# Optimization experiments

Measured on AMD Instinct MI355X. Metric: run time of the kernel, lower is better.

Reference implementation:

```python
import jax, jax.numpy as jnp
import numpy as np

TRIANGLE_TABLE = jnp.array([
    [-1,-1,-1,-1,-1,-1],[1,0,2,-1,-1,-1],[4,0,3,-1,-1,-1],[1,4,2,1,3,4],
    [3,1,5,-1,-1,-1],[2,3,0,2,5,3],[1,4,0,1,5,4],[4,2,5,-1,-1,-1],
    [4,5,2,-1,-1,-1],[4,1,0,4,5,1],[3,2,0,3,5,2],[1,3,5,-1,-1,-1],
    [4,1,2,4,3,1],[3,0,4,-1,-1,-1],[2,0,1,-1,-1,-1],[-1,-1,-1,-1,-1,-1]], dtype=jnp.int32)
NUM_TRI_TABLE = jnp.array([0,1,1,2,1,2,2,1,1,2,2,1,2,1,1,0], dtype=jnp.int32)
BASE_TET_EDGES = jnp.array([0,1,0,2,0,3,1,2,1,3,2,3], dtype=jnp.int32)
N_VERTS, N_TETS = 200_000, 1_000_000


def setup_inputs() -> dict:
    key = jax.random.key(0)
    k1, k2, k3 = jax.random.split(key, 3)
    pos_nx3 = jax.random.normal(k1, (N_VERTS, 3), jnp.float32)
    sdf_n = jax.random.normal(k2, (N_VERTS,), jnp.float32)
    tet_fx4 = jax.random.randint(k3, (N_TETS, 4), 0, N_VERTS, dtype=jnp.int32)
    return {"pos_nx3": pos_nx3, "sdf_n": sdf_n, "tet_fx4": tet_fx4}


def _mt_indices(sdf_n, tet_fx4):
    # Index-only part (torch.no_grad in the original). Dynamic shapes -> eager jax.
    occ_n = sdf_n > 0                              # [N]
    occ_fx4 = occ_n[tet_fx4]                       # [T,4]
    occ_sum = occ_fx4.sum(-1)
    valid = (occ_sum > 0) & (occ_sum < 4)          # surface-crossing tets
    tets_v = tet_fx4[valid]                        # [Tv,4]
    occ_v = occ_fx4[valid]
    # 6 edges per tet, sorted so (min,max) -> dedup identical to torch sort_edges+unique
    all_edges = jnp.sort(tets_v[:, BASE_TET_EDGES].reshape(-1, 2), axis=1)  # [Tv*6,2]
    unique_edges, idx_map = jnp.unique(all_edges, axis=0, return_inverse=True)
    idx_map = idx_map.reshape(-1)
    mask_edges = occ_n[unique_edges].sum(-1) == 1  # exactly one endpoint inside
    # compacting map: -1 for non-crossing edges, running index for crossing ones
    mapping = jnp.where(mask_edges, jnp.cumsum(mask_edges.astype(jnp.int32)) - 1, -1)
    idx_map = mapping[idx_map].reshape(-1, 6)      # [Tv,6] per-tet edge->vertex ids
    interp_v = unique_edges[mask_edges]            # [Ne,2] endpoint indices
    return valid, occ_v, idx_map, interp_v


def _interp_verts(pos, sdf, interp_v):
    e_pos = pos[interp_v]                                   # [Ne,2,3]
    e_sdf = sdf[interp_v] * jnp.array([1.0, -1.0], sdf.dtype)  # [s0,-s1]
    denom = e_sdf.sum(1, keepdims=True)                     # s0 - s1
    w = e_sdf[:, ::-1] / denom                              # [-s1, s0] / (s0-s1)
    return (e_pos * w[..., None]).sum(1)                    # [Ne,3]


def _map_uv(face_gidx, max_idx):
    Ngrid = int(np.ceil(np.sqrt((max_idx + 1) // 2)))
    lin = jnp.linspace(0.0, 1.0 - 1.0 / Ngrid, Ngrid, dtype=jnp.float32)
    tex_y, tex_x = jnp.meshgrid(lin, lin, indexing='ij')
    pad = 0.9 / Ngrid
    uvs = jnp.stack([tex_x, tex_y, tex_x + pad, tex_y,
                     tex_x + pad, tex_y + pad, tex_x, tex_y + pad], axis=-1).reshape(-1, 2)
    tet_raw = face_gidx // 2
    tet_idx = (tet_raw // Ngrid) * Ngrid + tet_raw % Ngrid
    tri_idx = face_gidx % 2
    uv_idx = jnp.stack([tet_idx * 4, tet_idx * 4 + tri_idx + 1,
                        tet_idx * 4 + tri_idx + 2], axis=-1).reshape(-1, 3)
    return uvs, uv_idx


def reference(pos_nx3, sdf_n, tet_fx4):
    valid, occ_v, idx_map, interp_v = _mt_indices(sdf_n, tet_fx4)
    verts = _interp_verts(pos_nx3, sdf_n, interp_v)
    # triangle-table lookup
    v_id = jnp.array([1, 2, 4, 8], jnp.int32)
    tetindex = (occ_v.astype(jnp.int32) * v_id).sum(-1)     # [Tv]
    num_tri = NUM_TRI_TABLE[tetindex]
    m1, m2 = num_tri == 1, num_tri == 2
    faces1 = jnp.take_along_axis(idx_map[m1], TRIANGLE_TABLE[tetindex[m1]][:, :3], axis=1).reshape(-1, 3)
    faces2 = jnp.take_along_axis(idx_map[m2], TRIANGLE_TABLE[tetindex[m2]][:, :6], axis=1).reshape(-1, 3)
    faces = jnp.concatenate([faces1, faces2], axis=0)
    tet_gidx = jnp.nonzero(valid)[0].astype(jnp.int32)
    face_gidx = jnp.concatenate([
        tet_gidx[m1] * 2,
        jnp.stack([tet_gidx[m2] * 2, tet_gidx[m2] * 2 + 1], axis=-1).reshape(-1)], axis=0)
    uvs, uv_idx = _map_uv(face_gidx, tet_fx4.shape[0] * 2)
    return verts, faces, uvs, uv_idx
```

## Files before the change

kernel.cpp:

```cpp
#include <hip/hip_runtime.h>
#include <cmath>

typedef unsigned long long u64;
typedef unsigned int u32;
typedef unsigned char u8;

#define SCAN_BLOCK 256
#define SCAN_ELEMS 8
#define SCAN_TILE (SCAN_BLOCK * SCAN_ELEMS)

#define BIN_SHIFT 9
#define BIN_VR 512
#define TETS_PER_BLOCK 2048

__constant__ int d_NUMTRI[16] = {0,1,1,2,1,2,2,1,1,2,2,1,2,1,1,0};
__constant__ int d_TRI[16][6] = {
 {-1,-1,-1,-1,-1,-1},{1,0,2,-1,-1,-1},{4,0,3,-1,-1,-1},{1,4,2,1,3,4},
 {3,1,5,-1,-1,-1},{2,3,0,2,5,3},{1,4,0,1,5,4},{4,2,5,-1,-1,-1},
 {4,5,2,-1,-1,-1},{4,1,0,4,5,1},{3,2,0,3,5,2},{1,3,5,-1,-1,-1},
 {4,1,2,4,3,1},{3,0,4,-1,-1,-1},{2,0,1,-1,-1,-1},{-1,-1,-1,-1,-1,-1}};
__constant__ int d_E0[6] = {0,0,0,1,1,2};
__constant__ int d_E1[6] = {1,2,3,2,3,3};

template <typename T>
__global__ void scanA_t(const T* in, T* out, int n, T* blockSums) {
    __shared__ T tsum[SCAN_BLOCK];
    int tbase = blockIdx.x * SCAN_TILE + threadIdx.x * SCAN_ELEMS;
    T vals[SCAN_ELEMS];
    T run = 0;
    for (int k = 0; k < SCAN_ELEMS; ++k) {
        int i = tbase + k;
        T v = (i < n) ? in[i] : (T)0;
        vals[k] = run;
        run += v;
    }
    tsum[threadIdx.x] = run;
    __syncthreads();
    for (int off = 1; off < SCAN_BLOCK; off <<= 1) {
        T v = (threadIdx.x >= (unsigned)off) ? tsum[threadIdx.x - off] : (T)0;
        __syncthreads();
        tsum[threadIdx.x] += v;
        __syncthreads();
    }
    T texcl = (threadIdx.x == 0) ? (T)0 : tsum[threadIdx.x - 1];
    for (int k = 0; k < SCAN_ELEMS; ++k) {
        int i = tbase + k;
        if (i < n) out[i] = texcl + vals[k];
    }
    if (threadIdx.x == SCAN_BLOCK - 1) blockSums[blockIdx.x] = tsum[SCAN_BLOCK - 1];
}

template <typename T>
__global__ void scanCf_t(T* out, int n, const T* bs, int nb, T* totalOut) {
    __shared__ T sh[2048];
    for (int i = threadIdx.x; i < 2048; i += 256) sh[i] = (i < nb) ? bs[i] : (T)0;
    __syncthreads();
    for (int off = 1; off < 2048; off <<= 1) {
        T v[8];
        for (int k = 0; k < 8; ++k) {
            int i = threadIdx.x + k * 256;
            v[k] = (i >= off) ? sh[i - off] : (T)0;
        }
        __syncthreads();
        for (int k = 0; k < 8; ++k) sh[threadIdx.x + k * 256] += v[k];
        __syncthreads();
    }
    if (totalOut && blockIdx.x == 0 && threadIdx.x == 0)
        *totalOut = (nb > 0) ? sh[nb - 1] : (T)0;
    T add = (blockIdx.x == 0) ? (T)0 : sh[blockIdx.x - 1];
    int base = blockIdx.x * SCAN_TILE;
    int end = base + SCAN_TILE; if (end > n) end = n;
    for (int i = base + threadIdx.x; i < end; i += SCAN_BLOCK) out[i] += add;
}

__global__ void k_scanA_dual(const u64* in64, u64* out64, int n64, u64* bs64,
                             const u32* in32, u32* out32, int n32, u32* bs32,
                             int nbT) {
    __shared__ u64 tsum[SCAN_BLOCK];
    if ((int)blockIdx.x < nbT) {
        int tbase = blockIdx.x * SCAN_TILE + threadIdx.x * SCAN_ELEMS;
        u64 vals[SCAN_ELEMS]; u64 run = 0;
        for (int k = 0; k < SCAN_ELEMS; ++k) {
            int i = tbase + k;
            u64 v = (i < n64) ? in64[i] : 0ull;
            vals[k] = run; run += v;
        }
        tsum[threadIdx.x] = run;
        __syncthreads();
        for (int off = 1; off < SCAN_BLOCK; off <<= 1) {
            u64 v = (threadIdx.x >= (unsigned)off) ? tsum[threadIdx.x - off] : 0ull;
            __syncthreads();
            tsum[threadIdx.x] += v;
            __syncthreads();
        }
        u64 texcl = (threadIdx.x == 0) ? 0ull : tsum[threadIdx.x - 1];
        for (int k = 0; k < SCAN_ELEMS; ++k) {
            int i = tbase + k;
            if (i < n64) out64[i] = texcl + vals[k];
        }
        if (threadIdx.x == SCAN_BLOCK - 1) bs64[blockIdx.x] = tsum[SCAN_BLOCK - 1];
    } else {
        int blk = (int)blockIdx.x - nbT;
        int tbase = blk * SCAN_TILE + threadIdx.x * SCAN_ELEMS;
        u32 vals[SCAN_ELEMS]; u32 run = 0;
        for (int k = 0; k < SCAN_ELEMS; ++k) {
            int i = tbase + k;
            u32 v = (i < n32) ? in32[i] : 0u;
            vals[k] = run; run += v;
        }
        tsum[threadIdx.x] = (u64)run;
        __syncthreads();
        for (int off = 1; off < SCAN_BLOCK; off <<= 1) {
            u64 v = (threadIdx.x >= (unsigned)off) ? tsum[threadIdx.x - off] : 0ull;
            __syncthreads();
            tsum[threadIdx.x] += v;
            __syncthreads();
        }
        u32 texcl = (threadIdx.x == 0) ? 0u : (u32)tsum[threadIdx.x - 1];
        for (int k = 0; k < SCAN_ELEMS; ++k) {
            int i = tbase + k;
            if (i < n32) out32[i] = texcl + vals[k];
        }
        if (threadIdx.x == SCAN_BLOCK - 1) bs32[blk] = (u32)tsum[SCAN_BLOCK - 1];
    }
}

__global__ void k_scanCf_dual(u64* out64, int n64, const u64* bs64, int nb64,
                              u64* total64,
                              u32* out32, int n32, const u32* bs32, int nb32,
                              u32* total32, int nbT) {
    __shared__ u64 sh[2048];
    if ((int)blockIdx.x < nbT) {
        for (int i = threadIdx.x; i < 2048; i += 256)
            sh[i] = (i < nb64) ? bs64[i] : 0ull;
        __syncthreads();
        for (int off = 1; off < 2048; off <<= 1) {
            u64 v[8];
            for (int k = 0; k < 8; ++k) {
                int i = threadIdx.x + k * 256;
                v[k] = (i >= off) ? sh[i - off] : 0ull;
            }
            __syncthreads();
            for (int k = 0; k < 8; ++k) sh[threadIdx.x + k * 256] += v[k];
            __syncthreads();
        }
        if (total64 && blockIdx.x == 0 && threadIdx.x == 0)
            *total64 = (nb64 > 0) ? sh[nb64 - 1] : 0ull;
        u64 add = (blockIdx.x == 0) ? 0ull : sh[blockIdx.x - 1];
        int base = blockIdx.x * SCAN_TILE;
        int end = base + SCAN_TILE; if (end > n64) end = n64;
        for (int i = base + threadIdx.x; i < end; i += SCAN_BLOCK) out64[i] += add;
    } else {
        int blk = (int)blockIdx.x - nbT;
        for (int i = threadIdx.x; i < 2048; i += 256)
            sh[i] = (i < nb32) ? (u64)bs32[i] : 0ull;
        __syncthreads();
        for (int off = 1; off < 2048; off <<= 1) {
            u64 v[8];
            for (int k = 0; k < 8; ++k) {
                int i = threadIdx.x + k * 256;
                v[k] = (i >= off) ? sh[i - off] : 0ull;
            }
            __syncthreads();
            for (int k = 0; k < 8; ++k) sh[threadIdx.x + k * 256] += v[k];
            __syncthreads();
        }
        if (total32 && blk == 0 && threadIdx.x == 0)
            *total32 = (nb32 > 0) ? (u32)sh[nb32 - 1] : 0u;
        u32 add = (blk == 0) ? 0u : (u32)sh[blk - 1];
        int base = blk * SCAN_TILE;
        int end = base + SCAN_TILE; if (end > n32) end = n32;
        for (int i = base + threadIdx.x; i < end; i += SCAN_BLOCK) out32[i] += add;
    }
}

__global__ __launch_bounds__(256) void k_classify_hist(
    const int* tet, const float* sdf, u8* ti8, u64* tetPack,
    u32* blockHist, u32* bigCnt, int T, int NB, int gB) {
    if (blockIdx.x == 0 && threadIdx.x == 0) *bigCnt = 0;
    __shared__ u32 hist[BIN_VR];
    for (int i = threadIdx.x; i < NB; i += 256) hist[i] = 0;
    __syncthreads();
    int base = blockIdx.x * TETS_PER_BLOCK;
    for (int it = 0; it < TETS_PER_BLOCK / 256; ++it) {
        int t = base + it * 256 + threadIdx.x;
        if (t < T) {
            int4 q = reinterpret_cast<const int4*>(tet)[t];
            int ti = (sdf[q.x] > 0.0f ? 1 : 0) | (sdf[q.y] > 0.0f ? 2 : 0) |
                     (sdf[q.z] > 0.0f ? 4 : 0) | (sdf[q.w] > 0.0f ? 8 : 0);
            ti8[t] = (u8)ti;
            int nt = d_NUMTRI[ti];
            tetPack[t] = ((u64)(nt == 1 ? 1 : 0) << 21) | (u64)(nt == 2 ? 1 : 0);
            if (nt != 0) {
                int idx[4] = {q.x, q.y, q.z, q.w};
                #pragma unroll
                for (int e = 0; e < 6; ++e) {
                    int e0 = d_E0[e], e1 = d_E1[e];
                    if (((ti >> e0) ^ (ti >> e1)) & 1) {
                        int a = idx[e0], b = idx[e1];
                        int mn = a < b ? a : b;
                        atomicAdd(&hist[mn >> BIN_SHIFT], 1u);
                    }
                }
            }
        }
    }
    __syncthreads();
    for (int i = threadIdx.x; i < NB; i += 256)
        blockHist[(size_t)i * gB + blockIdx.x] = hist[i];
}

__global__ __launch_bounds__(256) void k_binfill(
    const int* tet, const u8* ti8, const u32* blockHistScan,
    u64* binRec, int T, int NB, int gB) {
    __shared__ u32 cur[BIN_VR];
    for (int i = threadIdx.x; i < NB; i += 256)
        cur[i] = blockHistScan[(size_t)i * gB + blockIdx.x];
    __syncthreads();
    int base = blockIdx.x * TETS_PER_BLOCK;
    for (int it = 0; it < TETS_PER_BLOCK / 256; ++it) {
        int t = base + it * 256 + threadIdx.x;
        if (t < T) {
            int ti = ti8[t];
            if (d_NUMTRI[ti] != 0) {
                int4 q = reinterpret_cast<const int4*>(tet)[t];
                int idx[4] = {q.x, q.y, q.z, q.w};
                #pragma unroll
                for (int e = 0; e < 6; ++e) {
                    int e0 = d_E0[e], e1 = d_E1[e];
                    if (((ti >> e0) ^ (ti >> e1)) & 1) {
                        int a = idx[e0], b = idx[e1];
                        int mn = a < b ? a : b;
                        int mx = a < b ? b : a;
                        u32 slot = atomicAdd(&cur[mn >> BIN_SHIFT], 1u);
                        u32 rec = ((u32)(mn & (BIN_VR - 1)) << 18) | (u32)mx;
                        u32 pv = 6u * (u32)t + (u32)e;
                        binRec[slot] = ((u64)pv << 32) | (u64)rec;
                    }
                }
            }
        }
    }
}

__global__ __launch_bounds__(256) void k_bincount2(
    const u32* blockHistScan, const u32* totalPtr, const u64* binRec,
    u32* bucketCnt, u32* bucketStart, u32* binTotals, int V, int NB, int gB) {
    int bin = blockIdx.x;
    __shared__ u32 hist[BIN_VR];
    __shared__ u32 sc[BIN_VR];
    for (int i = threadIdx.x; i < BIN_VR; i += 256) hist[i] = 0;
    __syncthreads();
    u32 s = blockHistScan[(size_t)bin * gB];
    u32 e = (bin + 1 < NB) ? blockHistScan[(size_t)(bin + 1) * gB] : *totalPtr;
    for (u32 i = s + threadIdx.x; i < e; i += 256)
        atomicAdd(&hist[((u32)binRec[i]) >> 18], 1u);
    __syncthreads();
    int t0 = threadIdx.x, t1 = threadIdx.x + 256;
    sc[t0] = (hist[t0] + 3u) & ~3u;
    sc[t1] = (hist[t1] + 3u) & ~3u;
    __syncthreads();
    for (int off = 1; off < BIN_VR; off <<= 1) {
        u32 v0 = (t0 >= off) ? sc[t0 - off] : 0u;
        u32 v1 = (t1 >= off) ? sc[t1 - off] : 0u;
        __syncthreads();
        sc[t0] += v0; sc[t1] += v1;
        __syncthreads();
    }
    int vbase = bin << BIN_SHIFT;
    for (int i = threadIdx.x; i < BIN_VR; i += 256) {
        int v = vbase + i;
        if (v < V) {
            u32 h = hist[i];
            bucketCnt[v] = h;
            bucketStart[v] = sc[i] - ((h + 3u) & ~3u);
        }
    }
    if (threadIdx.x == 0) binTotals[bin] = sc[BIN_VR - 1];
}

__global__ __launch_bounds__(256) void k_binscatter2(
    const u32* blockHistScan, const u32* totalPtr, const u64* binRec,
    const u32* binTotals, u32* bucketStart, uint2* rec2,
    int V, int NB, int gB) {
    int bin = blockIdx.x;
    __shared__ u32 bt[BIN_VR];
    __shared__ u32 cur[BIN_VR];
    int t0 = threadIdx.x, t1 = threadIdx.x + 256;
    bt[t0] = (t0 < NB) ? binTotals[t0] : 0u;
    bt[t1] = (t1 < NB) ? binTotals[t1] : 0u;
    __syncthreads();
    for (int off = 1; off < BIN_VR; off <<= 1) {
        u32 v0 = (t0 >= off) ? bt[t0 - off] : 0u;
        u32 v1 = (t1 >= off) ? bt[t1 - off] : 0u;
        __syncthreads();
        bt[t0] += v0; bt[t1] += v1;
        __syncthreads();
    }
    u32 binBase = (bin == 0) ? 0u : bt[bin - 1];
    int vbase = bin << BIN_SHIFT;
    for (int i = threadIdx.x; i < BIN_VR; i += 256) {
        int v = vbase + i;
        if (v < V) {
            u32 a = binBase + bucketStart[v];
            bucketStart[v] = a;
            cur[i] = a;
        } else cur[i] = 0u;
    }
    __syncthreads();
    u32 s = blockHistScan[(size_t)bin * gB];
    u32 e = (bin + 1 < NB) ? blockHistScan[(size_t)(bin + 1) * gB] : *totalPtr;
    for (u32 i = s + threadIdx.x; i < e; i += 256) {
        u64 r = binRec[i];
        u32 rec = (u32)r;
        u32 pv = (u32)(r >> 32);
        u32 slot = atomicAdd(&cur[rec >> 18], 1u);
        rec2[slot] = make_uint2(rec & 0x3FFFFu, pv);
    }
}

__global__ __launch_bounds__(256) void k_sortdedup(
    const u32* bucketCnt, const u32* bucketStart, uint2* rec2,
    u8* idxmap, u32* crossCnt, u32* bigList, u32* bigCnt, int V)
{
    int v = blockIdx.x * 4 + (threadIdx.x >> 6);
    if (v >= V) return;
    int lane = threadIdx.x & 63;
    int n = (int)bucketCnt[v];
    if (n == 0) { if (lane == 0) crossCnt[v] = 0; return; }
    if (n > 64) {
        if (lane == 0) bigList[atomicAdd(bigCnt, 1u)] = (u32)v;
        return;
    }
    long long start = (long long)bucketStart[v];
    uint2 rp = (lane < n) ? rec2[start + lane] : make_uint2(0xFFFFFFFFu, 0u);
    u32 key = rp.x, prov = rp.y;
    int rank = 0;
    for (int j = 0; j < n; ++j) {
        u32 kj = (u32)__shfl((int)key, j);
        rank += (kj < key || (kj == key && j < lane)) ? 1 : 0;
    }
    u32 sorted = (u32)__builtin_amdgcn_ds_permute(rank << 2, (int)key);
    u32 prev = (u32)__shfl((int)sorted, lane - 1);
    bool nf = (lane < n) && (lane == 0 || prev != sorted);
    u64 m = __ballot(nf);
    int idx = __popcll(m & ((1ull << lane) - 1ull));
    if (nf) rec2[start + idx].x = sorted;
    int ldSorted = nf ? idx : idx - 1;
    int ldOrig = __shfl(ldSorted, rank);
    if (lane < n) idxmap[prov] = (u8)ldOrig;
    if (lane == 0) crossCnt[v] = (u32)__popcll(m);
}

__global__ __launch_bounds__(256) void k_sortbig(
    const u32* bigList, const u32* bigCnt, const u32* bucketCnt,
    const u32* bucketStart, uint2* rec2, u8* idxmap, u32* crossCnt)
{
    int nbig = (int)*bigCnt;
    int lane = threadIdx.x & 63;
    int wave = (blockIdx.x << 2) + (threadIdx.x >> 6);
    int stride = gridDim.x << 2;
    for (int b = wave; b < nbig; b += stride) {
        int v = (int)bigList[b];
        int n = (int)bucketCnt[v];
        long long start = (long long)bucketStart[v];
        if (n <= 256) {
            int chunks = (n + 63) >> 6;
            u32 key[4], prov[4], kf[4];
            int myi[4];
            #pragma unroll
            for (int c = 0; c < 4; ++c) {
                myi[c] = (c << 6) + lane;
                key[c] = 0xFFFFFFFFu; prov[c] = 0u;
                if (c < chunks && myi[c] < n) {
                    uint2 rp = rec2[start + myi[c]];
                    key[c] = rp.x; prov[c] = rp.y;
                }
            }
            bool tie[4] = {false, false, false, false};
            #pragma unroll
            for (int c2 = 0; c2 < 4; ++c2) {
                if (c2 < chunks) {
                    int base2 = c2 << 6;
                    int lim = n - base2; if (lim > 64) lim = 64;
                    for (int j = 0; j < lim; ++j) {
                        u32 kj = (u32)__shfl((int)key[c2], j);
                        int jg = base2 + j;
                        #pragma unroll
                        for (int c = 0; c < 4; ++c) {
                            if (c < chunks)
                                tie[c] = tie[c] | (kj == key[c] && jg < myi[c]);
                        }
                    }
                }
            }
            u32 uq = 0;
            #pragma unroll
            for (int c = 0; c < 4; ++c) {
                bool isf = (c < chunks) && (myi[c] < n) && !tie[c];
                kf[c] = key[c] | (isf ? 0x80000000u : 0u);
                u64 bal = __ballot(isf);
                uq += (u32)__popcll(bal);
            }
            int uless[4] = {0, 0, 0, 0};
            #pragma unroll
            for (int c2 = 0; c2 < 4; ++c2) {
                if (c2 < chunks) {
                    int base2 = c2 << 6;
                    int lim = n - base2; if (lim > 64) lim = 64;
                    for (int j = 0; j < lim; ++j) {
                        u32 kfj = (u32)__shfl((int)kf[c2], j);
                        u32 kj = kfj & 0x7FFFFFFFu;
                        bool fj = (kfj & 0x80000000u) != 0u;
                        #pragma unroll
                        for (int c = 0; c < 4; ++c) {
                            if (c < chunks)
                                uless[c] += (fj && kj < key[c]) ? 1 : 0;
                        }
                    }
                }
            }
            #pragma unroll
            for (int c = 0; c < 4; ++c) {
                if (c < chunks && myi[c] < n) {
                    if (kf[c] & 0x80000000u)
                        rec2[start + uless[c]].x = key[c];
                    idxmap[prov[c]] = (u8)uless[c];
                }
            }
            if (lane == 0) crossCnt[v] = uq;
        } else if (lane == 0) {
            for (int i = 1; i < n; ++i) {
                uint2 kk = rec2[start + i];
                int j = i - 1;
                while (j >= 0 && rec2[start + j].x > kk.x) {
                    rec2[start + j + 1] = rec2[start + j]; --j;
                }
                rec2[start + j + 1] = kk;
            }
            int uc = 0; u32 prev = 0xFFFFFFFFu;
            for (int i = 0; i < n; ++i) {
                uint2 r = rec2[start + i];
                if (r.x != prev) { rec2[start + uc].x = r.x; ++uc; prev = r.x; }
                idxmap[r.y] = (u8)(uc - 1);
            }
            crossCnt[v] = (u32)uc;
        }
    }
}

__global__ __launch_bounds__(256) void k_verts(
    const u32* crossCnt, const u32* bucketStart, const uint2* rec2, const u32* crossScan,
    const float* pos, const float* sdf, float* out, int V)
{
    int v = blockIdx.x * 8 + (threadIdx.x >> 5);
    if (v >= V) return;
    int slane = threadIdx.x & 31;
    int u = (int)crossCnt[v];
    if (u == 0) return;
    long long start = (long long)bucketStart[v];
    int cBase = (int)crossScan[v];
    float s0 = sdf[v];
    float p0x = pos[3 * v], p0y = pos[3 * v + 1], p0z = pos[3 * v + 2];
    for (int i = slane; i < u; i += 32) {
        int b = (int)rec2[start + i].x;
        long long k = cBase + i;
        float s1 = sdf[b];
        float d = s0 - s1;
        float w0 = -s1 / d, w1 = s0 / d;
        out[3 * k + 0] = p0x * w0 + pos[3 * b + 0] * w1;
        out[3 * k + 1] = p0y * w0 + pos[3 * b + 1] * w1;
        out[3 * k + 2] = p0z * w0 + pos[3 * b + 2] * w1;
    }
}

__global__ void k_faces(const int* tet, const u8* ti8, const u64* tetScan,
                        const u8* idxmap, const u32* crossScan,
                        const u64* meta0, const u32* NePtr,
                        float* out, int T, int Ngrid, long long uvFloats)
{
    int t = blockIdx.x * 256 + threadIdx.x;
    int uvTotal = Ngrid * Ngrid;
    if (t >= T && t >= uvTotal) return;

    u64 tot = *meta0;
    int C1 = (int)((tot >> 21) & 0x1fffffull);
    int C2 = (int)(tot & 0x1fffffull);
    int Ne = (int)*NePtr;
    long long facesBase = 3LL * Ne;
    long long F = (long long)C1 + 2LL * C2;
    long long uvBase = facesBase + 3LL * F;
    long long uvIdxBase = uvBase + uvFloats;

    if (t < uvTotal) {
        int i = t / Ngrid, j = t % Ngrid;
        double step = (Ngrid > 1) ? (1.0 - 1.0 / (double)Ngrid) / (double)(Ngrid - 1) : 0.0;
        float x = (float)((double)j * step);
        float y = (float)((double)i * step);
        float pad = (float)(0.9 / (double)Ngrid);
        long long o = uvBase + 8LL * t;
        out[o + 0] = x;       out[o + 1] = y;
        out[o + 2] = x + pad; out[o + 3] = y;
        out[o + 4] = x + pad; out[o + 5] = y + pad;
        out[o + 6] = x;       out[o + 7] = y + pad;
    }
    if (t >= T) return;

    int ti = ti8[t];
    int nt = d_NUMTRI[ti];
    if (nt == 0) return;

    int4 q = reinterpret_cast<const int4*>(tet)[t];
    int idx[4] = {q.x, q.y, q.z, q.w};
    const unsigned short* imp =
        reinterpret_cast<const unsigned short*>(idxmap + 6ll * t);
    unsigned short w0 = imp[0], w1 = imp[1], w2 = imp[2];
    u32 im[6] = {(u32)(w0 & 0xFF), (u32)(w0 >> 8),
                 (u32)(w1 & 0xFF), (u32)(w1 >> 8),
                 (u32)(w2 & 0xFF), (u32)(w2 >> 8)};
    const int* row = d_TRI[ti];

    int emap[6];
    unsigned done = 0;
    float fv[6];
    #pragma unroll
    for (int j = 0; j < 6; ++j) {
        if (j >= 3 * nt) break;
        int e = row[j];
        if (!((done >> e) & 1)) {
            done |= 1u << e;
            int a = idx[d_E0[e]], b = idx[d_E1[e]];
            if (b < a) a = b;
            emap[e] = (int)crossScan[a] + (int)im[e];
        }
        fv[j] = (float)emap[e];
    }

    u64 sc = tetScan[t];
    int r1s = (int)((sc >> 21) & 0x1fffffull);
    int r2s = (int)(sc & 0x1fffffull);
    int tet_idx = (t / Ngrid) * Ngrid + (t % Ngrid);

    if (nt == 1) {
        long long f = r1s;
        out[facesBase + 3 * f + 0] = fv[0];
        out[facesBase + 3 * f + 1] = fv[1];
        out[facesBase + 3 * f + 2] = fv[2];
        out[uvIdxBase + 3 * f + 0] = (float)(4 * tet_idx);
        out[uvIdxBase + 3 * f + 1] = (float)(4 * tet_idx + 1);
        out[uvIdxBase + 3 * f + 2] = (float)(4 * tet_idx + 2);
    } else {
        long long f0 = (long long)C1 + 2LL * r2s;
        out[facesBase + 3 * f0 + 0] = fv[0];
        out[facesBase + 3 * f0 + 1] = fv[1];
        out[facesBase + 3 * f0 + 2] = fv[2];
        out[facesBase + 3 * (f0 + 1) + 0] = fv[3];
        out[facesBase + 3 * (f0 + 1) + 1] = fv[4];
        out[facesBase + 3 * (f0 + 1) + 2] = fv[5];
        out[uvIdxBase + 3 * f0 + 0] = (float)(4 * tet_idx);
        out[uvIdxBase + 3 * f0 + 1] = (float)(4 * tet_idx + 1);
        out[uvIdxBase + 3 * f0 + 2] = (float)(4 * tet_idx + 2);
        out[uvIdxBase + 3 * (f0 + 1) + 0] = (float)(4 * tet_idx);
        out[uvIdxBase + 3 * (f0 + 1) + 1] = (float)(4 * tet_idx + 2);
        out[uvIdxBase + 3 * (f0 + 1) + 2] = (float)(4 * tet_idx + 3);
    }
}

template <typename T>
static void run_scan2(const T* in, T* out, int n, T* blockSums, T* totalOut,
                      hipStream_t stream) {
    int nb = (n + SCAN_TILE - 1) / SCAN_TILE;
    scanA_t<T><<<nb, SCAN_BLOCK, 0, stream>>>(in, out, n, blockSums);
    scanCf_t<T><<<nb, SCAN_BLOCK, 0, stream>>>(out, n, blockSums, nb, totalOut);
}

extern "C" void kernel_launch(void* const* d_in, const int* in_sizes, int n_in,
                              void* d_out, int out_size, void* d_ws, size_t ws_size,
                              hipStream_t stream) {
    const float* pos = (const float*)d_in[0];
    const float* sdf = (const float*)d_in[1];
    const int* tet = (const int*)d_in[2];
    int V = in_sizes[1];
    int T = in_sizes[2] / 4;
    float* out = (float*)d_out;

    int NB = (V + BIN_VR - 1) / BIN_VR;
    int gB = (T + TETS_PER_BLOCK - 1) / TETS_PER_BLOCK;
    int nHist = NB * gB;

    char* p = (char*)d_ws;
    auto alloc = [&](size_t bytes) -> void* {
        void* r = (void*)p;
        p += (bytes + 255) & ~(size_t)255;
        return r;
    };
    u8*  ti8           = (u8*) alloc((size_t)T);
    u64* tetPack       = (u64*)alloc((size_t)T * 8);
    u64* tetScan       = (u64*)alloc((size_t)T * 8);
    u32* blockHist     = (u32*)alloc((size_t)nHist * 4);
    u32* blockHistScan = (u32*)alloc((size_t)nHist * 4);
    u64* binRec        = (u64*)alloc((size_t)6 * T * 8);
    u32* bucketCnt     = (u32*)alloc((size_t)V * 4);
    u32* bucketStart   = (u32*)alloc((size_t)V * 4);
    u32* binTotals     = (u32*)alloc((size_t)BIN_VR * 4);
    u32* crossCnt      = (u32*)alloc((size_t)V * 4);
    u32* crossScan     = (u32*)alloc((size_t)V * 4);
    uint2* rec2        = (uint2*)alloc(((size_t)6 * T + 4 * (size_t)V) * 8);
    u32* bigList       = (u32*)alloc((size_t)V * 4);
    u64* blockSums64   = (u64*)alloc(2048 * 8);
    u32* blockSums32   = (u32*)alloc(2048 * 4);
    u64* meta64        = (u64*)alloc(8 * 8);
    u32* NePtr         = (u32*)(meta64 + 4);
    u32* NeInstPtr     = (u32*)(meta64 + 5);
    u32* bigCnt        = (u32*)(meta64 + 6);

    u8* idxmap = (u8*)binRec;

    long long M = (2LL * T + 1) / 2;
    int Ngrid = (int)std::sqrt((double)M);
    while ((long long)Ngrid * Ngrid < M) ++Ngrid;
    if (Ngrid < 1) Ngrid = 1;
    long long uvFloats = 8LL * Ngrid * Ngrid;

    int gV4 = (V + 3) / 4;
    int gV8 = (V + 7) / 8;
    long long fw = (long long)Ngrid * Ngrid;
    if (fw < (long long)T) fw = T;
    int gFU = (int)((fw + 255) / 256);

    int nbT = (T + SCAN_TILE - 1) / SCAN_TILE;
    int nbH = (nHist + SCAN_TILE - 1) / SCAN_TILE;

    k_classify_hist<<<gB, 256, 0, stream>>>(tet, sdf, ti8, tetPack, blockHist,
                                            bigCnt, T, NB, gB);
    k_scanA_dual<<<nbT + nbH, SCAN_BLOCK, 0, stream>>>(
        tetPack, tetScan, T, blockSums64,
        blockHist, blockHistScan, nHist, blockSums32, nbT);
    k_scanCf_dual<<<nbT + nbH, SCAN_BLOCK, 0, stream>>>(
        tetScan, T, blockSums64, nbT, meta64,
        blockHistScan, nHist, blockSums32, nbH, NeInstPtr, nbT);
    k_binfill<<<gB, 256, 0, stream>>>(tet, ti8, blockHistScan, binRec,
                                      T, NB, gB);
    k_bincount2<<<NB, 256, 0, stream>>>(blockHistScan, NeInstPtr, binRec,
                                        bucketCnt, bucketStart, binTotals,
                                        V, NB, gB);
    k_binscatter2<<<NB, 256, 0, stream>>>(blockHistScan, NeInstPtr, binRec,
                                          binTotals, bucketStart, rec2,
                                          V, NB, gB);
    k_sortdedup<<<gV4, 256, 0, stream>>>(bucketCnt, bucketStart, rec2,
                                         idxmap, crossCnt, bigList, bigCnt, V);
    k_sortbig<<<1024, 256, 0, stream>>>(bigList, bigCnt, bucketCnt, bucketStart,
                                        rec2, idxmap, crossCnt);
    run_scan2<u32>(crossCnt, crossScan, V, blockSums32, NePtr, stream);
    k_verts<<<gV8, 256, 0, stream>>>(crossCnt, bucketStart, rec2, crossScan,
                                     pos, sdf, out, V);
    k_faces<<<gFU, 256, 0, stream>>>(tet, ti8, tetScan, idxmap, crossScan,
                                     meta64, NePtr, out, T, Ngrid, uvFloats);
}
```

Baseline: 423.6 us.

## Fuse bin count and bin scatter into one kernel using bin-local offsets

```diff
diff --git a/kernel.cpp b/kernel.cpp
--- a/kernel.cpp
+++ b/kernel.cpp
@@ -243,12 +243,13 @@
     }
 }
 
-__global__ __launch_bounds__(256) void k_bincount2(
+__global__ __launch_bounds__(256) void k_binsort(
     const u32* blockHistScan, const u32* totalPtr, const u64* binRec,
-    u32* bucketCnt, u32* bucketStart, u32* binTotals, int V, int NB, int gB) {
+    u32* bucketCnt, u32* bucketStart, uint2* rec2, int V, int NB, int gB) {
     int bin = blockIdx.x;
     __shared__ u32 hist[BIN_VR];
     __shared__ u32 sc[BIN_VR];
+    __shared__ u32 cur[BIN_VR];
     for (int i = threadIdx.x; i < BIN_VR; i += 256) hist[i] = 0;
     __syncthreads();
     u32 s = blockHistScan[(size_t)bin * gB];
@@ -257,8 +258,8 @@
         atomicAdd(&hist[((u32)binRec[i]) >> 18], 1u);
     __syncthreads();
     int t0 = threadIdx.x, t1 = threadIdx.x + 256;
-    sc[t0] = (hist[t0] + 3u) & ~3u;
-    sc[t1] = (hist[t1] + 3u) & ~3u;
+    sc[t0] = hist[t0];
+    sc[t1] = hist[t1];
     __syncthreads();
     for (int off = 1; off < BIN_VR; off <<= 1) {
         u32 v0 = (t0 >= off) ? sc[t0 - off] : 0u;
@@ -270,46 +271,15 @@
     int vbase = bin << BIN_SHIFT;
     for (int i = threadIdx.x; i < BIN_VR; i += 256) {
         int v = vbase + i;
+        u32 h = hist[i];
+        u32 abs0 = s + sc[i] - h;
         if (v < V) {
-            u32 h = hist[i];
             bucketCnt[v] = h;
-            bucketStart[v] = sc[i] - ((h + 3u) & ~3u);
-        }
-    }
-    if (threadIdx.x == 0) binTotals[bin] = sc[BIN_VR - 1];
-}
-
-__global__ __launch_bounds__(256) void k_binscatter2(
-    const u32* blockHistScan, const u32* totalPtr, const u64* binRec,
-    const u32* binTotals, u32* bucketStart, uint2* rec2,
-    int V, int NB, int gB) {
-    int bin = blockIdx.x;
-    __shared__ u32 bt[BIN_VR];
-    __shared__ u32 cur[BIN_VR];
-    int t0 = threadIdx.x, t1 = threadIdx.x + 256;
-    bt[t0] = (t0 < NB) ? binTotals[t0] : 0u;
-    bt[t1] = (t1 < NB) ? binTotals[t1] : 0u;
-    __syncthreads();
-    for (int off = 1; off < BIN_VR; off <<= 1) {
-        u32 v0 = (t0 >= off) ? bt[t0 - off] : 0u;
-        u32 v1 = (t1 >= off) ? bt[t1 - off] : 0u;
-        __syncthreads();
-        bt[t0] += v0; bt[t1] += v1;
-        __syncthreads();
-    }
-    u32 binBase = (bin == 0) ? 0u : bt[bin - 1];
-    int vbase = bin << BIN_SHIFT;
-    for (int i = threadIdx.x; i < BIN_VR; i += 256) {
-        int v = vbase + i;
-        if (v < V) {
-            u32 a = binBase + bucketStart[v];
-            bucketStart[v] = a;
-            cur[i] = a;
-        } else cur[i] = 0u;
-    }
-    __syncthreads();
-    u32 s = blockHistScan[(size_t)bin * gB];
-    u32 e = (bin + 1 < NB) ? blockHistScan[(size_t)(bin + 1) * gB] : *totalPtr;
+            bucketStart[v] = abs0;
+        }
+        cur[i] = abs0;
+    }
+    __syncthreads();
     for (u32 i = s + threadIdx.x; i < e; i += 256) {
         u64 r = binRec[i];
         u32 rec = (u32)r;
@@ -602,7 +572,6 @@
     u64* binRec        = (u64*)alloc((size_t)6 * T * 8);
     u32* bucketCnt     = (u32*)alloc((size_t)V * 4);
     u32* bucketStart   = (u32*)alloc((size_t)V * 4);
-    u32* binTotals     = (u32*)alloc((size_t)BIN_VR * 4);
     u32* crossCnt      = (u32*)alloc((size_t)V * 4);
     u32* crossScan     = (u32*)alloc((size_t)V * 4);
     uint2* rec2        = (uint2*)alloc(((size_t)6 * T + 4 * (size_t)V) * 8);
@@ -641,12 +610,8 @@
         blockHistScan, nHist, blockSums32, nbH, NeInstPtr, nbT);
     k_binfill<<<gB, 256, 0, stream>>>(tet, ti8, blockHistScan, binRec,
                                       T, NB, gB);
-    k_bincount2<<<NB, 256, 0, stream>>>(blockHistScan, NeInstPtr, binRec,
-                                        bucketCnt, bucketStart, binTotals,
-                                        V, NB, gB);
-    k_binscatter2<<<NB, 256, 0, stream>>>(blockHistScan, NeInstPtr, binRec,
-                                          binTotals, bucketStart, rec2,
-                                          V, NB, gB);
+    k_binsort<<<NB, 256, 0, stream>>>(blockHistScan, NeInstPtr, binRec,
+                                      bucketCnt, bucketStart, rec2, V, NB, gB);
     k_sortdedup<<<gV4, 256, 0, stream>>>(bucketCnt, bucketStart, rec2,
                                          idxmap, crossCnt, bigList, bigCnt, V);
     k_sortbig<<<1024, 256, 0, stream>>>(bigList, bigCnt, bucketCnt, bucketStart,
```

New measurement: 411.0 us. 3.0% less time.
